# Optimization experiments

Measured on AMD Instinct MI355X. Metric: run time of the kernel, lower is better.

Reference implementation:

```python
import jax, jax.numpy as jnp
import numpy as np

N_NODES = 50000
N_EDGES = 600000
IN_C = 128
HID = 128
OUT_C = 32
N_GRAPHS = 64


def setup_inputs() -> dict:
    key = jax.random.key(0)
    ks = jax.random.split(key, 12)
    x = jax.random.normal(ks[0], (N_NODES, IN_C), dtype=jnp.float32)
    edge_index = jax.random.randint(ks[1], (2, N_EDGES), 0, N_NODES, dtype=jnp.int64)
    batch = jnp.sort(jax.random.randint(ks[2], (N_NODES,), 0, N_GRAPHS, dtype=jnp.int64))
    s1 = 1.0 / np.sqrt(IN_C)
    s2 = 1.0 / np.sqrt(HID)
    # SAGEConv: out = lin_l(mean_neighbors) + lin_r(x); lin_l has bias, lin_r has none
    W1l = jax.random.uniform(ks[3], (HID, IN_C), minval=-s1, maxval=s1, dtype=jnp.float32)
    b1 = jax.random.uniform(ks[4], (HID,), minval=-s1, maxval=s1, dtype=jnp.float32)
    W1r = jax.random.uniform(ks[5], (HID, IN_C), minval=-s1, maxval=s1, dtype=jnp.float32)
    W2l = jax.random.uniform(ks[6], (HID, HID), minval=-s2, maxval=s2, dtype=jnp.float32)
    b2 = jax.random.uniform(ks[7], (HID,), minval=-s2, maxval=s2, dtype=jnp.float32)
    W2r = jax.random.uniform(ks[8], (HID, HID), minval=-s2, maxval=s2, dtype=jnp.float32)
    Wlin = jax.random.uniform(ks[9], (OUT_C, HID), minval=-s2, maxval=s2, dtype=jnp.float32)
    blin = jax.random.uniform(ks[10], (OUT_C,), minval=-s2, maxval=s2, dtype=jnp.float32)
    return {"x": x, "edge_index": edge_index, "batch": batch,
            "W1l": W1l, "b1": b1, "W1r": W1r,
            "W2l": W2l, "b2": b2, "W2r": W2r,
            "Wlin": Wlin, "blin": blin}


def _sage_conv(x, src, dst, Wl, bl, Wr):
    # mean aggregation of source-node features onto destination nodes
    msg_sum = jax.ops.segment_sum(x[src], dst, num_segments=N_NODES)  # [N, d]
    deg = jax.ops.segment_sum(jnp.ones((src.shape[0],), x.dtype), dst, num_segments=N_NODES)
    mean = msg_sum / jnp.maximum(deg, 1.0)[:, None]
    return mean @ Wl.T + bl + x @ Wr.T


def reference(x, edge_index, batch, W1l, b1, W1r, W2l, b2, W2r, Wlin, blin):
    src, dst = edge_index[0], edge_index[1]
    h = jax.nn.relu(_sage_conv(x, src, dst, W1l, b1, W1r))
    h = jax.nn.relu(_sage_conv(h, src, dst, W2l, b2, W2r))
    # global mean pool over graph ids
    gsum = jax.ops.segment_sum(h, batch, num_segments=N_GRAPHS)        # [G, HID]
    cnt = jax.ops.segment_sum(jnp.ones((h.shape[0],), h.dtype), batch, num_segments=N_GRAPHS)
    pooled = gsum / jnp.maximum(cnt, 1.0)[:, None]
    return pooled @ Wlin.T + blin
```

## Files before the change

### kernel.cpp

```cpp
#include <hip/hip_runtime.h>
#include <hip/hip_fp16.h>

#define N_NODES 50000
#define N_EDGES 600000
#define N_GRAPHS 64
#define HID 128
#define OUT_C 32

#define N_SCAN_BLOCKS ((N_NODES + 255) / 256)
#define SCAN_FLAG 0x40000000

typedef __attribute__((ext_vector_type(8))) _Float16 half8;
typedef __attribute__((ext_vector_type(4))) float f32x4;

#define ZERO_INTS (N_GRAPHS * 128 + N_NODES + N_SCAN_BLOCKS)

__global__ __launch_bounds__(256) void prep_kernel(
    const float* __restrict__ x, const int* __restrict__ batch,
    const float* __restrict__ W1l, const float* __restrict__ W1r,
    const float* __restrict__ W2l, const float* __restrict__ W2r,
    __half* __restrict__ xh, __half* __restrict__ Wt1, __half* __restrict__ Wt2,
    int* __restrict__ zero_base, int* __restrict__ gstart) {
    const int b = blockIdx.x;
    const int t = threadIdx.x;
    const int gtid = b * 256 + t;
    const int gsz = gridDim.x * 256;
    for (int i = gtid; i < ZERO_INTS; i += gsz) zero_base[i] = 0;

    for (int i = gtid; i <= N_NODES; i += gsz) {
        if (i == 0) {
            int b1 = batch[0];
            for (int g = 0; g <= b1; ++g) gstart[g] = 0;
        } else if (i == N_NODES) {
            int b0 = batch[N_NODES - 1];
            for (int g = b0 + 1; g <= N_GRAPHS; ++g) gstart[g] = N_NODES;
        } else {
            int b0 = batch[i - 1], b1 = batch[i];
            for (int g = b0 + 1; g <= b1; ++g) gstart[g] = i;
        }
    }

    if (b < 16) {
        for (int i = gtid; i < 65536; i += 4096) {
            int which = i >> 15;
            int j = i & 32767;
            int n = j >> 8, k = j & 255;
            const float* Wl = which ? W2l : W1l;
            const float* Wr = which ? W2r : W1r;
            float a = (k < 128) ? Wl[n * 128 + k] : Wr[n * 128 + (k - 128)];
            (which ? Wt2 : Wt1)[j] = __float2half(a);
        }
    } else {
        int i = ((b - 16) * 256 + t) * 4;
        if (i < N_NODES * 128) {
            float4 v = *(const float4*)(x + i);
            __half2 a = __floats2half2_rn(v.x, v.y);
            __half2 c = __floats2half2_rn(v.z, v.w);
            uint2 st;
            st.x = *(const unsigned int*)&a;
            st.y = *(const unsigned int*)&c;
            *(uint2*)(xh + i) = st;
        }
    }
}

__global__ void deg_kernel(const int* __restrict__ dst, int* __restrict__ deg, int E) {
    int e = blockIdx.x * 256 + threadIdx.x;
    if (e < E) atomicAdd(&deg[dst[e]], 1);
}

__global__ __launch_bounds__(256) void scan_fused(
    const int* __restrict__ deg, int* __restrict__ bsum,
    int* __restrict__ rowptr, int* __restrict__ cursor, float* __restrict__ invdeg) {
    __shared__ int s[256];
    const int b = blockIdx.x;
    const int t = threadIdx.x;
    const int idx = b * 256 + t;
    const int v = (idx < N_NODES) ? deg[idx] : 0;
    s[t] = v;
    __syncthreads();
    for (int off = 1; off < 256; off <<= 1) {
        int u = (t >= off) ? s[t - off] : 0;
        __syncthreads();
        s[t] += u;
        __syncthreads();
    }
    const int incl = s[t];
    if (t == 255) atomicExch(&bsum[b], incl | SCAN_FLAG);

    int pv = 0;
    if (t < b) {
        int w;
        do { w = atomicAdd(&bsum[t], 0); } while (!(w & SCAN_FLAG));
        pv = w & ~SCAN_FLAG;
    }
    __syncthreads();
    s[t] = pv;
    __syncthreads();
    for (int off = 128; off > 0; off >>= 1) {
        if (t < off) s[t] += s[t + off];
        __syncthreads();
    }
    const int boffs = s[0];

    if (idx < N_NODES) {
        int rp = boffs + incl - v;
        rowptr[idx] = rp;
        cursor[idx] = rp;
        invdeg[idx] = 1.0f / fmaxf((float)v, 1.0f);
    }
    if (b == N_SCAN_BLOCKS - 1 && t == 255) rowptr[N_NODES] = boffs + incl;
}

__global__ void fill_kernel(const int* __restrict__ src, const int* __restrict__ dst,
                            int* __restrict__ cursor, int* __restrict__ eidx, int E) {
    int e = blockIdx.x * 256 + threadIdx.x;
    if (e < E) {
        int pos = atomicAdd(&cursor[dst[e]], 1);
        eidx[pos] = src[e];
    }
}

#define AGG8(vv, aa, ab) { aa.x += (float)vv[0]; aa.y += (float)vv[1]; \
                           aa.z += (float)vv[2]; aa.w += (float)vv[3]; \
                           ab.x += (float)vv[4]; ab.y += (float)vv[5]; \
                           ab.z += (float)vv[6]; ab.w += (float)vv[7]; }

__global__ __launch_bounds__(256) void aggregate_f16(
    const __half* __restrict__ feat16, const int* __restrict__ rowptr,
    const int* __restrict__ eidx, const float* __restrict__ invdeg,
    __half* __restrict__ mean16) {
    const int wave = threadIdx.x >> 6;
    const int lane = threadIdx.x & 63;
    const int nh   = lane >> 4;
    const int sub  = lane & 15;
    const int node = blockIdx.x * 16 + wave * 4 + nh;
    const bool act = (node < N_NODES);
    int beg = 0, end = 0;
    if (act) { beg = rowptr[node]; end = rowptr[node + 1]; }
    const size_t coff = (size_t)sub * 8;

    float4 a0 = {0.f,0.f,0.f,0.f}, b0 = {0.f,0.f,0.f,0.f};
    float4 a1 = {0.f,0.f,0.f,0.f}, b1 = {0.f,0.f,0.f,0.f};
    float4 a2 = {0.f,0.f,0.f,0.f}, b2 = {0.f,0.f,0.f,0.f};
    float4 a3 = {0.f,0.f,0.f,0.f}, b3 = {0.f,0.f,0.f,0.f};
    int i = beg;
    for (; i + 8 <= end; i += 8) {
        int s0 = eidx[i+0], s1 = eidx[i+1], s2 = eidx[i+2], s3 = eidx[i+3];
        int s4 = eidx[i+4], s5 = eidx[i+5], s6 = eidx[i+6], s7 = eidx[i+7];
        half8 v0 = *(const half8*)(feat16 + (size_t)s0 * 128 + coff);
        half8 v1 = *(const half8*)(feat16 + (size_t)s1 * 128 + coff);
        half8 v2 = *(const half8*)(feat16 + (size_t)s2 * 128 + coff);
        half8 v3 = *(const half8*)(feat16 + (size_t)s3 * 128 + coff);
        half8 v4 = *(const half8*)(feat16 + (size_t)s4 * 128 + coff);
        half8 v5 = *(const half8*)(feat16 + (size_t)s5 * 128 + coff);
        half8 v6 = *(const half8*)(feat16 + (size_t)s6 * 128 + coff);
        half8 v7 = *(const half8*)(feat16 + (size_t)s7 * 128 + coff);
        AGG8(v0, a0, b0); AGG8(v1, a1, b1); AGG8(v2, a2, b2); AGG8(v3, a3, b3);
        AGG8(v4, a0, b0); AGG8(v5, a1, b1); AGG8(v6, a2, b2); AGG8(v7, a3, b3);
    }
    if (i + 4 <= end) {
        int s0 = eidx[i+0], s1 = eidx[i+1], s2 = eidx[i+2], s3 = eidx[i+3];
        half8 v0 = *(const half8*)(feat16 + (size_t)s0 * 128 + coff);
        half8 v1 = *(const half8*)(feat16 + (size_t)s1 * 128 + coff);
        half8 v2 = *(const half8*)(feat16 + (size_t)s2 * 128 + coff);
        half8 v3 = *(const half8*)(feat16 + (size_t)s3 * 128 + coff);
        AGG8(v0, a0, b0); AGG8(v1, a1, b1); AGG8(v2, a2, b2); AGG8(v3, a3, b3);
        i += 4;
    }
    if (i + 2 <= end) {
        int s0 = eidx[i+0], s1 = eidx[i+1];
        half8 v0 = *(const half8*)(feat16 + (size_t)s0 * 128 + coff);
        half8 v1 = *(const half8*)(feat16 + (size_t)s1 * 128 + coff);
        AGG8(v0, a0, b0); AGG8(v1, a1, b1);
        i += 2;
    }
    if (i < end) {
        int s0 = eidx[i];
        half8 v0 = *(const half8*)(feat16 + (size_t)s0 * 128 + coff);
        AGG8(v0, a0, b0);
    }

    if (act) {
        const float sc = invdeg[node];
        half8 r;
        r[0] = (_Float16)(((a0.x + a1.x) + (a2.x + a3.x)) * sc);
        r[1] = (_Float16)(((a0.y + a1.y) + (a2.y + a3.y)) * sc);
        r[2] = (_Float16)(((a0.z + a1.z) + (a2.z + a3.z)) * sc);
        r[3] = (_Float16)(((a0.w + a1.w) + (a2.w + a3.w)) * sc);
        r[4] = (_Float16)(((b0.x + b1.x) + (b2.x + b3.x)) * sc);
        r[5] = (_Float16)(((b0.y + b1.y) + (b2.y + b3.y)) * sc);
        r[6] = (_Float16)(((b0.z + b1.z) + (b2.z + b3.z)) * sc);
        r[7] = (_Float16)(((b0.w + b1.w) + (b2.w + b3.w)) * sc);
        *(half8*)(mean16 + (size_t)node * 128 + coff) = r;
    }
}

#define GBM 64
#define BPAD 8

__global__ __launch_bounds__(256) void sage_gemm_f16(
    const __half* __restrict__ mean16, const __half* __restrict__ feat16,
    const __half* __restrict__ Wt, const float* __restrict__ bias,
    const int* __restrict__ batch, __half* __restrict__ out16,
    float* __restrict__ pooled, int M) {
    __shared__ __align__(16) __half Bs[128][256 + BPAD];
    __shared__ float pool_lds[8][128];

    const int tid = threadIdx.x;
    const int wave = tid >> 6;
    const int lane = tid & 63;
    const int l15 = lane & 15;
    const int quad = lane >> 4;
    const int row0 = blockIdx.x * GBM;
    const int gi_a = min(row0 + wave * 16 + l15, M - 1);

    for (int id = tid; id < 128 * 32; id += 256) {
        int n = id >> 5;
        int kc = (id & 31) * 8;
        *(half8*)&Bs[n][kc] = *(const half8*)(Wt + (size_t)n * 256 + kc);
    }
    if (pooled) {
        for (int i = tid; i < 8 * 128; i += 256) pool_lds[i >> 7][i & 127] = 0.f;
    }

    half8 af[8];
#pragma unroll
    for (int kb = 0; kb < 8; ++kb) {
        const int k0 = kb * 32;
        const __half* ap = (k0 < 128)
            ? (mean16 + (size_t)gi_a * 128 + k0 + quad * 8)
            : (feat16 + (size_t)gi_a * 128 + (k0 - 128) + quad * 8);
        af[kb] = *(const half8*)ap;
    }

    f32x4 acc[8];
#pragma unroll
    for (int t = 0; t < 8; ++t) acc[t] = (f32x4){0.f, 0.f, 0.f, 0.f};

    __syncthreads();

#pragma unroll
    for (int kb = 0; kb < 8; ++kb) {
#pragma unroll
        for (int t = 0; t < 8; ++t) {
            const half8 b = *(const half8*)&Bs[t * 16 + l15][kb * 32 + quad * 8];
            acc[t] = __builtin_amdgcn_mfma_f32_16x16x32_f16(af[kb], b, acc[t], 0, 0, 0);
        }
    }

    if (pooled) {
        const int gmin = batch[row0];
#pragma unroll
        for (int r = 0; r < 4; ++r) {
            int gi = row0 + wave * 16 + quad * 4 + r;
            if (gi < M) {
                int gl = batch[gi] - gmin;
#pragma unroll
                for (int t = 0; t < 8; ++t) {
                    int col = t * 16 + l15;
                    float v = fmaxf(acc[t][r] + bias[col], 0.f);
                    if (gl < 8) atomicAdd(&pool_lds[gl][col], v);
                    else        atomicAdd(&pooled[(gmin + gl) * 128 + col], v);
                }
            }
        }
        __syncthreads();
        for (int i = tid; i < 8 * 128; i += 256) {
            int gl = i >> 7, c = i & 127;
            float v = pool_lds[gl][c];
            if (v != 0.f) atomicAdd(&pooled[(gmin + gl) * 128 + c], v);
        }
    } else {
#pragma unroll
        for (int r = 0; r < 4; ++r) {
            int gi = row0 + wave * 16 + quad * 4 + r;
            if (gi < M) {
#pragma unroll
                for (int t = 0; t < 8; ++t) {
                    int col = t * 16 + l15;
                    float v = fmaxf(acc[t][r] + bias[col], 0.f);
                    out16[(size_t)gi * 128 + col] = __float2half(v);
                }
            }
        }
    }
}

__global__ void final_kernel(const float* __restrict__ pooled,
                             const int* __restrict__ gstart,
                             const float* __restrict__ Wlin, const float* __restrict__ blin,
                             float* __restrict__ out) {
    int g = blockIdx.x;
    int j = threadIdx.x;
    float inv = 1.0f / fmaxf((float)(gstart[g + 1] - gstart[g]), 1.0f);
    float sum = blin[j];
    const float* w = Wlin + j * 128;
    const float* p = pooled + (size_t)g * 128;
    for (int c = 0; c < 128; ++c) sum += p[c] * inv * w[c];
    out[g * 32 + j] = sum;
}

extern "C" void kernel_launch(void* const* d_in, const int* in_sizes, int n_in,
                              void* d_out, int out_size, void* d_ws, size_t ws_size,
                              hipStream_t stream) {
    const float* x    = (const float*)d_in[0];
    const int*   src  = (const int*)d_in[1];
    const int*   dst  = ((const int*)d_in[1]) + N_EDGES;
    const int*   batch= (const int*)d_in[2];
    const float* W1l  = (const float*)d_in[3];
    const float* b1   = (const float*)d_in[4];
    const float* W1r  = (const float*)d_in[5];
    const float* W2l  = (const float*)d_in[6];
    const float* b2   = (const float*)d_in[7];
    const float* W2r  = (const float*)d_in[8];
    const float* Wlin = (const float*)d_in[9];
    const float* blin = (const float*)d_in[10];
    float* out = (float*)d_out;

    __half* xh     = (__half*)d_ws;
    __half* mean16 = xh + 6400000;
    __half* h1_16  = mean16 + 6400000;
    __half* Wt1    = h1_16 + 6400000;
    __half* Wt2    = Wt1 + 32768;
    float* invdeg  = (float*)(Wt2 + 32768);
    int*   gstart  = (int*)(invdeg + N_NODES);
    float* pooled  = (float*)(gstart + 65);
    int*   degi    = (int*)(pooled + N_GRAPHS * 128);
    int*   bsum    = degi + N_NODES;
    int*   cursor  = bsum + N_SCAN_BLOCKS;
    int*   rowptr  = cursor + N_NODES;
    int*   eidx    = rowptr + N_NODES + 1;

    prep_kernel<<<16 + (N_NODES * 128 / 4 + 255) / 256, 256, 0, stream>>>(
        x, batch, W1l, W1r, W2l, W2r, xh, Wt1, Wt2, (int*)pooled, gstart);

    deg_kernel<<<(N_EDGES + 255) / 256, 256, 0, stream>>>(dst, degi, N_EDGES);
    scan_fused<<<N_SCAN_BLOCKS, 256, 0, stream>>>(degi, bsum, rowptr, cursor, invdeg);
    fill_kernel<<<(N_EDGES + 255) / 256, 256, 0, stream>>>(src, dst, cursor, eidx, N_EDGES);

    const int gemm_grid = (N_NODES + GBM - 1) / GBM;
    const int agg_grid = (N_NODES + 15) / 16;

    aggregate_f16<<<agg_grid, 256, 0, stream>>>(xh, rowptr, eidx, invdeg, mean16);
    sage_gemm_f16<<<gemm_grid, 256, 0, stream>>>(mean16, xh, Wt1, b1, batch,
                                                 h1_16, (float*)nullptr, N_NODES);

    aggregate_f16<<<agg_grid, 256, 0, stream>>>(h1_16, rowptr, eidx, invdeg, mean16);
    sage_gemm_f16<<<gemm_grid, 256, 0, stream>>>(mean16, h1_16, Wt2, b2, batch,
                                                 (__half*)nullptr, pooled, N_NODES);

    final_kernel<<<N_GRAPHS, 32, 0, stream>>>(pooled, gstart, Wlin, blin, out);
}
```

Baseline: 282.4 us.

## Process two row tiles per GEMM block and prefetch next A fragments

Each sage_gemm block now handles two consecutive 64-row tiles instead of one, reusing the weight tile already staged in LDS. While the current tile computes, the next tile's A fragments are loaded into registers. This halves the number of LDS weight-staging passes and pool-flush passes. In exchange the grid shrinks by half, which lowers occupancy and parallelism on a large GPU, and register pressure rises from the extra fragment buffer.

```diff
diff --git a/kernel.cpp b/kernel.cpp
--- a/kernel.cpp
+++ b/kernel.cpp
@@ -197,6 +197,7 @@
 }
 
 #define GBM 64
+#define MTILES 2
 #define BPAD 8
 
 __global__ __launch_bounds__(256) void sage_gemm_f16(
@@ -212,8 +213,7 @@
     const int lane = tid & 63;
     const int l15 = lane & 15;
     const int quad = lane >> 4;
-    const int row0 = blockIdx.x * GBM;
-    const int gi_a = min(row0 + wave * 16 + l15, M - 1);
+    const int row_base = blockIdx.x * (GBM * MTILES);
 
     for (int id = tid; id < 128 * 32; id += 256) {
         int n = id >> 5;
@@ -225,64 +225,91 @@
     }
 
     half8 af[8];
-#pragma unroll
-    for (int kb = 0; kb < 8; ++kb) {
-        const int k0 = kb * 32;
-        const __half* ap = (k0 < 128)
-            ? (mean16 + (size_t)gi_a * 128 + k0 + quad * 8)
-            : (feat16 + (size_t)gi_a * 128 + (k0 - 128) + quad * 8);
-        af[kb] = *(const half8*)ap;
-    }
-
-    f32x4 acc[8];
-#pragma unroll
-    for (int t = 0; t < 8; ++t) acc[t] = (f32x4){0.f, 0.f, 0.f, 0.f};
+    {
+        const int gi0 = min(row_base + wave * 16 + l15, M - 1);
+#pragma unroll
+        for (int kb = 0; kb < 8; ++kb) {
+            const int k0 = kb * 32;
+            const __half* ap = (k0 < 128)
+                ? (mean16 + (size_t)gi0 * 128 + k0 + quad * 8)
+                : (feat16 + (size_t)gi0 * 128 + (k0 - 128) + quad * 8);
+            af[kb] = *(const half8*)ap;
+        }
+    }
 
     __syncthreads();
 
-#pragma unroll
-    for (int kb = 0; kb < 8; ++kb) {
-#pragma unroll
-        for (int t = 0; t < 8; ++t) {
-            const half8 b = *(const half8*)&Bs[t * 16 + l15][kb * 32 + quad * 8];
-            acc[t] = __builtin_amdgcn_mfma_f32_16x16x32_f16(af[kb], b, acc[t], 0, 0, 0);
-        }
-    }
-
-    if (pooled) {
-        const int gmin = batch[row0];
-#pragma unroll
-        for (int r = 0; r < 4; ++r) {
-            int gi = row0 + wave * 16 + quad * 4 + r;
-            if (gi < M) {
-                int gl = batch[gi] - gmin;
-#pragma unroll
-                for (int t = 0; t < 8; ++t) {
-                    int col = t * 16 + l15;
-                    float v = fmaxf(acc[t][r] + bias[col], 0.f);
-                    if (gl < 8) atomicAdd(&pool_lds[gl][col], v);
-                    else        atomicAdd(&pooled[(gmin + gl) * 128 + col], v);
+    const int gmin = pooled ? batch[min(row_base, M - 1)] : 0;
+
+    for (int t2 = 0; t2 < MTILES; ++t2) {
+        const int row0 = row_base + t2 * GBM;
+
+        half8 afn[8];
+        if (t2 + 1 < MTILES) {
+            const int gin = min(row0 + GBM + wave * 16 + l15, M - 1);
+#pragma unroll
+            for (int kb = 0; kb < 8; ++kb) {
+                const int k0 = kb * 32;
+                const __half* ap = (k0 < 128)
+                    ? (mean16 + (size_t)gin * 128 + k0 + quad * 8)
+                    : (feat16 + (size_t)gin * 128 + (k0 - 128) + quad * 8);
+                afn[kb] = *(const half8*)ap;
+            }
+        }
+
+        f32x4 acc[8];
+#pragma unroll
+        for (int t = 0; t < 8; ++t) acc[t] = (f32x4){0.f, 0.f, 0.f, 0.f};
+
+#pragma unroll
+        for (int kb = 0; kb < 8; ++kb) {
+#pragma unroll
+            for (int t = 0; t < 8; ++t) {
+                const half8 b = *(const half8*)&Bs[t * 16 + l15][kb * 32 + quad * 8];
+                acc[t] = __builtin_amdgcn_mfma_f32_16x16x32_f16(af[kb], b, acc[t], 0, 0, 0);
+            }
+        }
+
+        if (pooled) {
+#pragma unroll
+            for (int r = 0; r < 4; ++r) {
+                int gi = row0 + wave * 16 + quad * 4 + r;
+                if (gi < M) {
+                    int gl = batch[gi] - gmin;
+#pragma unroll
+                    for (int t = 0; t < 8; ++t) {
+                        int col = t * 16 + l15;
+                        float v = fmaxf(acc[t][r] + bias[col], 0.f);
+                        if (gl < 8) atomicAdd(&pool_lds[gl][col], v);
+                        else        atomicAdd(&pooled[(gmin + gl) * 128 + col], v);
+                    }
                 }
             }
-        }
+        } else {
+#pragma unroll
+            for (int r = 0; r < 4; ++r) {
+                int gi = row0 + wave * 16 + quad * 4 + r;
+                if (gi < M) {
+#pragma unroll
+                    for (int t = 0; t < 8; ++t) {
+                        int col = t * 16 + l15;
+                        float v = fmaxf(acc[t][r] + bias[col], 0.f);
+                        out16[(size_t)gi * 128 + col] = __float2half(v);
+                    }
+                }
+            }
+        }
+
+#pragma unroll
+        for (int kb = 0; kb < 8; ++kb) af[kb] = afn[kb];
+    }
+
+    if (pooled) {
         __syncthreads();
         for (int i = tid; i < 8 * 128; i += 256) {
             int gl = i >> 7, c = i & 127;
             float v = pool_lds[gl][c];
             if (v != 0.f) atomicAdd(&pooled[(gmin + gl) * 128 + c], v);
-        }
-    } else {
-#pragma unroll
-        for (int r = 0; r < 4; ++r) {
-            int gi = row0 + wave * 16 + quad * 4 + r;
-            if (gi < M) {
-#pragma unroll
-                for (int t = 0; t < 8; ++t) {
-                    int col = t * 16 + l15;
-                    float v = fmaxf(acc[t][r] + bias[col], 0.f);
-                    out16[(size_t)gi * 128 + col] = __float2half(v);
-                }
-            }
         }
     }
 }
@@ -339,7 +366,7 @@
     scan_fused<<<N_SCAN_BLOCKS, 256, 0, stream>>>(degi, bsum, rowptr, cursor, invdeg);
     fill_kernel<<<(N_EDGES + 255) / 256, 256, 0, stream>>>(src, dst, cursor, eidx, N_EDGES);
 
-    const int gemm_grid = (N_NODES + GBM - 1) / GBM;
+    const int gemm_grid = (N_NODES + GBM * MTILES - 1) / (GBM * MTILES);
     const int agg_grid = (N_NODES + 15) / 16;
 
     aggregate_f16<<<agg_grid, 256, 0, stream>>>(xh, rowptr, eidx, invdeg, mean16);
```

New measurement: 281.0 us. About the same (-0.5%).
